# Optimization experiments

Measured on AMD Instinct MI355X. Metric: run time of the kernel, lower is better.

## Reference

```python
import jax, jax.numpy as jnp
import numpy as np


def _lstm_layer(x, Wih, Whh, bih, bhh):
    # x: (B, S, I); Wih: (4H, I); Whh: (4H, H)
    B, S, _ = x.shape
    H = Whh.shape[1]
    # Big batched GEMM for all input projections at once.
    xproj = jnp.einsum('bsi,gi->bsg', x, Wih) + bih + bhh  # (B, S, 4H)
    xproj_t = jnp.transpose(xproj, (1, 0, 2))              # (S, B, 4H)

    def step(carry, xp):
        h, c = carry
        gates = xp + h @ Whh.T                             # (B, 4H)
        i, f, g, o = jnp.split(gates, 4, axis=-1)          # torch gate order i,f,g,o
        i = jax.nn.sigmoid(i)
        f = jax.nn.sigmoid(f)
        g = jnp.tanh(g)
        o = jax.nn.sigmoid(o)
        c = f * c + i * g
        h = o * jnp.tanh(c)
        return (h, c), h

    h0 = jnp.zeros((B, H), dtype=x.dtype)
    c0 = jnp.zeros((B, H), dtype=x.dtype)
    (_, _), hs = jax.lax.scan(step, (h0, c0), xproj_t)     # hs: (S, B, H)
    return jnp.transpose(hs, (1, 0, 2))                    # (B, S, H)


def setup_inputs() -> dict:
    key = jax.random.key(0)
    ks = jax.random.split(key, 12)
    B, S, I, H, O = 64, 512, 512, 1024, 64
    s_in = 1.0 / np.sqrt(H)
    inp = {
        'x': jax.random.normal(ks[0], (B, S, I), dtype=jnp.float32),
        'Wih0': jax.random.uniform(ks[1], (4 * H, I), minval=-s_in, maxval=s_in),
        'Whh0': jax.random.uniform(ks[2], (4 * H, H), minval=-s_in, maxval=s_in),
        'bih0': jax.random.uniform(ks[3], (4 * H,), minval=-s_in, maxval=s_in),
        'bhh0': jax.random.uniform(ks[4], (4 * H,), minval=-s_in, maxval=s_in),
        'Wih1': jax.random.uniform(ks[5], (4 * H, H), minval=-s_in, maxval=s_in),
        'Whh1': jax.random.uniform(ks[6], (4 * H, H), minval=-s_in, maxval=s_in),
        'bih1': jax.random.uniform(ks[7], (4 * H,), minval=-s_in, maxval=s_in),
        'bhh1': jax.random.uniform(ks[8], (4 * H,), minval=-s_in, maxval=s_in),
        'Wfc': jax.random.uniform(ks[9], (O, H), minval=-s_in, maxval=s_in),
        'bfc': jax.random.uniform(ks[10], (O,), minval=-s_in, maxval=s_in),
    }
    return inp


def reference(x, Wih0, Whh0, bih0, bhh0, Wih1, Whh1, bih1, bhh1, Wfc, bfc):
    h = _lstm_layer(x, Wih0, Whh0, bih0, bhh0)   # (B, S, H)
    h = _lstm_layer(h, Wih1, Whh1, bih1, bhh1)   # (B, S, H)
    # dropout = 0.0 (eval mode) -> identity
    logits = jnp.einsum('bsh,oh->bso', h, Wfc) + bfc  # (B, S, O)
    return logits
```

## Files before the change

### kernel.cpp

```cpp
#include <hip/hip_runtime.h>
#include <stdint.h>

typedef _Float16 f16;
typedef _Float16 f16x8 __attribute__((ext_vector_type(8)));
typedef float f32x4 __attribute__((ext_vector_type(4)));

#define MFMA16(a, b, c) __builtin_amdgcn_mfma_f32_16x16x32_f16((a), (b), (c), 0, 0, 0)



__global__ void k_conv_x(const float* __restrict__ x, f16* __restrict__ x16) {
  int i = blockIdx.x * 256 + threadIdx.x;
  int o = i * 8;
  int s = o >> 15, b = (o >> 9) & 63, c = o & 511;
  const float* src = x + (size_t)b * 262144 + (size_t)s * 512 + c;
  float4 v0 = *(const float4*)(src);
  float4 v1 = *(const float4*)(src + 4);
  union { f16 h[8]; f16x8 v; } t;
  t.h[0] = (f16)v0.x; t.h[1] = (f16)v0.y; t.h[2] = (f16)v0.z; t.h[3] = (f16)v0.w;
  t.h[4] = (f16)v1.x; t.h[5] = (f16)v1.y; t.h[6] = (f16)v1.z; t.h[7] = (f16)v1.w;
  *(f16x8*)(x16 + o) = t.v;
}

__global__ void k_conv_wfrag(const float* __restrict__ Wih, const float* __restrict__ Whh,
                             f16* __restrict__ Wf, int KI, int KK, int kPer) {
  int fid = blockIdx.x;
  int lane = threadIdx.x;
  int cf = fid & 1; int rest = fid >> 1;
  int kk = rest % KK; rest /= KK; int w = rest & 7; int jb = rest >> 3;
  int c = cf * 16 + (lane & 15);
  int g = (c >> 3) * 1024 + jb * 8 + (c & 7);
  int k = w * kPer + kk * 32 + ((lane >> 4) << 3);
  const float* src = (k < KI) ? (Wih + (size_t)g * KI + k)
                              : (Whh + (size_t)g * 1024 + (k - KI));
  union { f16 h[8]; f16x8 v; } t;
#pragma unroll
  for (int i = 0; i < 8; ++i) t.h[i] = (f16)src[i];
  *(f16x8*)(Wf + ((size_t)fid * 64 + lane) * 8) = t.v;
}

__global__ void k_conv_bias(const float* __restrict__ bih, const float* __restrict__ bhh,
                            float* __restrict__ br) {
  int d = blockIdx.x * 64 + threadIdx.x;
  int jb = d >> 5, r = d & 31;
  int g = (r >> 3) * 1024 + jb * 8 + (r & 7);
  br[d] = bih[g] + bhh[g];
}

__global__ void k_conv_wfc(const float* __restrict__ Wfc, f16* __restrict__ Wfc16) {
  int i = blockIdx.x * 256 + threadIdx.x;
  Wfc16[i] = (f16)Wfc[i];
}

__global__ __launch_bounds__(512, 2)
void k_persist(const f16* __restrict__ x16,
               const f16* __restrict__ W0f, const float* __restrict__ b0r,
               const f16* __restrict__ W1f, const float* __restrict__ b1r,
               f16* __restrict__ h0buf, f16* __restrict__ h1buf,
               f16* __restrict__ h1all, int* flags, int* gflags) {
  const int layer = blockIdx.x >> 7;
  const int jb = blockIdx.x & 127;

  __shared__ float cred[8][64][36];

  int* flag0 = flags;
  int* flag1 = flags + 4096;
  int* myflag = (layer ? flag1 : flag0) + jb * 32;

  const int tid = threadIdx.x;
  const int w = tid >> 6, lane = tid & 63;
  const int l15 = lane & 15, q8 = (lane >> 4) << 3;
  const int m = tid >> 3, jl = tid & 7, jg = jb * 8 + jl;

  const float* bias = (layer ? b1r : b0r) + jb * 32;
  const float bI = bias[jl], bF = bias[8 + jl], bG = bias[16 + jl], bO = bias[24 + jl];
  float creg = 0.f;

  const int* gp = gflags + l15;
  const bool isg1 = l15 >= 8;
  const int* aggp = (layer ? flag1 : flag0) + (jb * 16 + l15) * 32;
  int* myg = gflags + (layer ? 8 : 0) + jb;

#define POLLG(n0v, n1v)                                                                  \
  {                                                                                      \
    int need_ = isg1 ? (n1v) : (n0v);                                                    \
    if (w == 0) {                                                                        \
      for (;;) {                                                                         \
        int v_ = __hip_atomic_load(gp, __ATOMIC_RELAXED, __HIP_MEMORY_SCOPE_AGENT);      \
        if (__all(v_ >= need_)) break;                                                   \
        __builtin_amdgcn_s_sleep(2);                                                     \
      }                                                                                  \
    }                                                                                    \
    __syncthreads();                                                                     \
  }

#define CRED_AND_POINTWISE(HOUT, HALL)                                                   \
  {                                                                                      \
    _Pragma("unroll") for (int rf = 0; rf < 4; ++rf)                                     \
      _Pragma("unroll") for (int cf = 0; cf < 2; ++cf)                                   \
        _Pragma("unroll") for (int r = 0; r < 4; ++r)                                    \
          cred[w][rf * 16 + (lane >> 4) * 4 + r][cf * 16 + l15] = acc[rf][cf][r];        \
    __syncthreads();                                                                     \
    float ip = bI, fp = bF, gp2 = bG, op = bO;                                           \
    _Pragma("unroll") for (int ww = 0; ww < 8; ++ww) {                                   \
      ip += cred[ww][m][jl];                                                             \
      fp += cred[ww][m][8 + jl];                                                         \
      gp2 += cred[ww][m][16 + jl];                                                       \
      op += cred[ww][m][24 + jl];                                                        \
    }                                                                                    \
    float ig = 1.f / (1.f + __expf(-ip));                                                \
    float fg = 1.f / (1.f + __expf(-fp));                                                \
    float ea = __expf(-2.f * fabsf(gp2));                                                \
    float gg = copysignf((1.f - ea) / (1.f + ea), gp2);                                  \
    float og = 1.f / (1.f + __expf(-op));                                                \
    creg = fg * creg + ig * gg;                                                          \
    float eb = __expf(-2.f * fabsf(creg));                                               \
    float hval = og * copysignf((1.f - eb) / (1.f + eb), creg);                          \
    size_t idx = (size_t)m * 1024 + jg;                                                  \
    union { f16 h; unsigned short s; } cv; cv.h = (f16)hval;                             \
    __hip_atomic_store((unsigned short*)((HOUT) + idx), cv.s,                            \
                       __ATOMIC_RELAXED, __HIP_MEMORY_SCOPE_AGENT);                      \
    if (HALL) ((f16*)(HALL))[idx] = cv.h;                                                \
    __syncthreads();                         \
    if (tid == 0)                                                                        \
      __hip_atomic_store(myflag, t + 1, __ATOMIC_RELAXED, __HIP_MEMORY_SCOPE_AGENT);     \
    if (jb < 8 && w == 0) {                                                              \
      for (;;) {                                                                         \
        int v_ = __hip_atomic_load(aggp, __ATOMIC_RELAXED, __HIP_MEMORY_SCOPE_AGENT);    \
        if (__all(v_ >= t + 1)) break;                                                   \
        __builtin_amdgcn_s_sleep(1);                                                     \
      }                                                                                  \
      if (lane == 0)                                                                     \
        __hip_atomic_store(myg, t + 1, __ATOMIC_RELAXED, __HIP_MEMORY_SCOPE_AGENT);      \
    }                                                                                    \
  }

#define GLD_X(dst, addr)                                                                 \
  asm volatile("global_load_dwordx4 %0, %1, off sc0 sc1" : "=&v"(dst) : "v"(addr) : "memory")
#define GLD_C(dst, addr)                                                                 \
  asm volatile("global_load_dwordx4 %0, %1, off" : "=&v"(dst) : "v"(addr) : "memory")
#define WAITV(n)                                                                         \
  { asm volatile("s_waitcnt vmcnt(" #n ")" ::: "memory"); __builtin_amdgcn_sched_barrier(0); }

  if (layer == 0) {
    const int KK = 6;
    f16x8 wreg[6][2];
#pragma unroll
    for (int kk = 0; kk < KK; ++kk)
#pragma unroll
      for (int cf = 0; cf < 2; ++cf)
        wreg[kk][cf] = *(const f16x8*)(W0f + ((size_t)((jb * 8 + w) * KK + kk) * 2 + cf) * 512 + lane * 8);
#pragma unroll
    for (int kk = 0; kk < KK; ++kk)
      asm volatile("" : "+v"(wreg[kk][0]), "+v"(wreg[kk][1]));

    const int kbeg = w * 192;
    for (int t = 0; t < 512; ++t) {
      const f16* A0 = x16 + (size_t)t * 32768;
      const f16* A1 = h0buf + (size_t)((t + 3) & 3) * 65536;
      f16* hout = h0buf + (size_t)(t & 3) * 65536;

      POLLG(t, t - 3);

      f16x8 af[4][4];
#define ISSUE0(kk)                                                                       \
      {                                                                                  \
        int k_ = kbeg + (kk) * 32 + q8;                                                  \
        if (k_ < 512) {                                                                  \
          const f16* ap_ = A0 + k_;                                                      \
          _Pragma("unroll") for (int rf = 0; rf < 4; ++rf)                               \
            GLD_C(af[(kk) & 3][rf], ap_ + (size_t)(rf * 16 + l15) * 512);                \
        } else {                                                                         \
          const f16* ap_ = A1 + (k_ - 512);                                              \
          _Pragma("unroll") for (int rf = 0; rf < 4; ++rf)                               \
            GLD_X(af[(kk) & 3][rf], ap_ + (size_t)(rf * 16 + l15) * 1024);               \
        }                                                                                \
      }
#define MF0(kk)                                                                          \
      { _Pragma("unroll") for (int rf = 0; rf < 4; ++rf) {                               \
          acc[rf][0] = MFMA16(af[(kk) & 3][rf], wreg[kk][0], acc[rf][0]);                \
          acc[rf][1] = MFMA16(af[(kk) & 3][rf], wreg[kk][1], acc[rf][1]); } }

      f32x4 acc[4][2];
#pragma unroll
      for (int i = 0; i < 4; ++i) {
        acc[i][0] = f32x4{0.f, 0.f, 0.f, 0.f};
        acc[i][1] = f32x4{0.f, 0.f, 0.f, 0.f};
      }

      ISSUE0(0) ISSUE0(1) ISSUE0(2) ISSUE0(3)
      WAITV(12) MF0(0) ISSUE0(4)
      WAITV(12) MF0(1) ISSUE0(5)
      WAITV(12) MF0(2)
      WAITV(8)  MF0(3)
      WAITV(4)  MF0(4)
      WAITV(0)  MF0(5)
#undef ISSUE0
#undef MF0

      CRED_AND_POINTWISE(hout, (f16*)nullptr);
    }
  } else {
    const int KK = 8;
    f16x8 wreg[8][2];
#pragma unroll
    for (int kk = 0; kk < KK; ++kk)
#pragma unroll
      for (int cf = 0; cf < 2; ++cf)
        wreg[kk][cf] = *(const f16x8*)(W1f + ((size_t)((jb * 8 + w) * KK + kk) * 2 + cf) * 512 + lane * 8);
#pragma unroll
    for (int kk = 0; kk < KK; ++kk)
      asm volatile("" : "+v"(wreg[kk][0]), "+v"(wreg[kk][1]));

    const int kbeg = w * 256;
    for (int t = 0; t < 512; ++t) {
      const f16* A0 = h0buf + (size_t)(t & 3) * 65536;
      const f16* A1 = h1buf + (size_t)((t + 3) & 3) * 65536;
      f16* hout = h1buf + (size_t)(t & 3) * 65536;
      f16* hall = h1all + (size_t)t * 65536;

      POLLG(t + 1, t);

      f16x8 af[4][4];
#define ISSUE1(kk)                                                                       \
      {                                                                                  \
        int k_ = kbeg + (kk) * 32 + q8;                                                  \
        const f16* ap_ = (k_ < 1024) ? (A0 + k_) : (A1 + (k_ - 1024));                   \
        _Pragma("unroll") for (int rf = 0; rf < 4; ++rf)                                 \
          GLD_X(af[(kk) & 3][rf], ap_ + (size_t)(rf * 16 + l15) * 1024);                 \
      }
#define MF1(kk)                                                                          \
      { _Pragma("unroll") for (int rf = 0; rf < 4; ++rf) {                               \
          acc[rf][0] = MFMA16(af[(kk) & 3][rf], wreg[kk][0], acc[rf][0]);                \
          acc[rf][1] = MFMA16(af[(kk) & 3][rf], wreg[kk][1], acc[rf][1]); } }

      f32x4 acc[4][2];
#pragma unroll
      for (int i = 0; i < 4; ++i) {
        acc[i][0] = f32x4{0.f, 0.f, 0.f, 0.f};
        acc[i][1] = f32x4{0.f, 0.f, 0.f, 0.f};
      }

      ISSUE1(0) ISSUE1(1) ISSUE1(2) ISSUE1(3)
      WAITV(12) MF1(0) ISSUE1(4)
      WAITV(12) MF1(1) ISSUE1(5)
      WAITV(12) MF1(2) ISSUE1(6)
      WAITV(12) MF1(3) ISSUE1(7)
      WAITV(12) MF1(4)
      WAITV(8)  MF1(5)
      WAITV(4)  MF1(6)
      WAITV(0)  MF1(7)
#undef ISSUE1
#undef MF1

      CRED_AND_POINTWISE(hout, hall);
    }
  }
#undef POLLG
#undef CRED_AND_POINTWISE
#undef GLD_X
#undef GLD_C
#undef WAITV
}

__global__ __launch_bounds__(512, 1)
void k_fc(const f16* __restrict__ h1all, const f16* __restrict__ Wfc16,
          const float* __restrict__ bfc, float* __restrict__ out) {
  const int s = blockIdx.x;
  const f16* A = h1all + (size_t)s * 65536;
  __shared__ float credf[8][64][68];

  const int w = threadIdx.x >> 6;
  const int lane = threadIdx.x & 63;
  const int l15 = lane & 15;
  const int ksub = (lane >> 4) << 3;

  f32x4 acc[4][4];
#pragma unroll
  for (int i = 0; i < 4; ++i)
#pragma unroll
    for (int j = 0; j < 4; ++j) acc[i][j] = f32x4{0.f, 0.f, 0.f, 0.f};

  const int kbeg = w * 128, kend = kbeg + 128;
  f16x8 af0[4], bf0[4], af1[4], bf1[4];

  auto LOADK = [&](int kc, f16x8(&a)[4], f16x8(&b)[4]) {
    const f16* ap = A + kc + ksub;
#pragma unroll
    for (int rf = 0; rf < 4; ++rf)
      a[rf] = *(const f16x8*)(ap + (size_t)(rf * 16 + l15) * 1024);
    const f16* bp = Wfc16 + kc + ksub;
#pragma unroll
    for (int cf = 0; cf < 4; ++cf)
      b[cf] = *(const f16x8*)(bp + (size_t)(cf * 16 + l15) * 1024);
  };

  LOADK(kbeg, af0, bf0);
  for (int kc = kbeg; kc < kend; kc += 64) {
    LOADK(kc + 32, af1, bf1);
#pragma unroll
    for (int rf = 0; rf < 4; ++rf)
#pragma unroll
      for (int cf = 0; cf < 4; ++cf) acc[rf][cf] = MFMA16(af0[rf], bf0[cf], acc[rf][cf]);
    if (kc + 64 < kend) LOADK(kc + 64, af0, bf0);
#pragma unroll
    for (int rf = 0; rf < 4; ++rf)
#pragma unroll
      for (int cf = 0; cf < 4; ++cf) acc[rf][cf] = MFMA16(af1[rf], bf1[cf], acc[rf][cf]);
  }

#pragma unroll
  for (int rf = 0; rf < 4; ++rf)
#pragma unroll
    for (int cf = 0; cf < 4; ++cf)
#pragma unroll
      for (int r = 0; r < 4; ++r)
        credf[w][rf * 16 + (lane >> 4) * 4 + r][cf * 16 + l15] = acc[rf][cf][r];

  __syncthreads();

  int m = threadIdx.x >> 3;
  int cbase = (threadIdx.x & 7) * 8;
#pragma unroll
  for (int u = 0; u < 8; ++u) {
    int col = cbase + u;
    float v = bfc[col];
#pragma unroll
    for (int ww = 0; ww < 8; ++ww) v += credf[ww][m][col];
    out[((size_t)m * 512 + s) * 64 + col] = v;
  }
}

extern "C" void kernel_launch(void* const* d_in, const int* in_sizes, int n_in,
                              void* d_out, int out_size, void* d_ws, size_t ws_size,
                              hipStream_t stream) {
  const float* x    = (const float*)d_in[0];
  const float* Wih0 = (const float*)d_in[1];
  const float* Whh0 = (const float*)d_in[2];
  const float* bih0 = (const float*)d_in[3];
  const float* bhh0 = (const float*)d_in[4];
  const float* Wih1 = (const float*)d_in[5];
  const float* Whh1 = (const float*)d_in[6];
  const float* bih1 = (const float*)d_in[7];
  const float* bhh1 = (const float*)d_in[8];
  const float* Wfc  = (const float*)d_in[9];
  const float* bfc  = (const float*)d_in[10];
  float* out = (float*)d_out;

  char* ws = (char*)d_ws;
  f16*   W0f   = (f16*)(ws + 0);
  f16*   W1f   = (f16*)(ws + 12582912);
  f16*   Wfc16 = (f16*)(ws + 29360128);
  float* b0r   = (float*)(ws + 29491200);
  float* b1r   = (float*)(ws + 29507584);
  f16*   x16   = (f16*)(ws + 29523968);
  f16*   h1all = (f16*)(ws + 63078400);
  f16*   h0buf = (f16*)(ws + 130187264);
  f16*   h1buf = (f16*)(ws + 130711552);
  int*   flags = (int*)(ws + 131235840);
  int*   gfl   = (int*)(ws + 131268608);

  k_conv_x<<<8192, 256, 0, stream>>>(x, x16);
  k_conv_wfrag<<<12288, 64, 0, stream>>>(Wih0, Whh0, W0f, 512, 6, 192);
  k_conv_wfrag<<<16384, 64, 0, stream>>>(Wih1, Whh1, W1f, 1024, 8, 256);
  k_conv_bias<<<64, 64, 0, stream>>>(bih0, bhh0, b0r);
  k_conv_bias<<<64, 64, 0, stream>>>(bih1, bhh1, b1r);
  k_conv_wfc<<<256, 256, 0, stream>>>(Wfc, Wfc16);
  hipMemsetAsync(ws + 130187264, 0, 524288 * 2 + 32768 + 64, stream);

  {
    const f16* x16c = x16; const f16* W0fc = W0f; const float* b0rc = b0r;
    const f16* W1fc = W1f; const float* b1rc = b1r;
    f16 *p0 = h0buf, *p1 = h1buf, *ph = h1all;
    int* fl = flags; int* gf = gfl;
    void* kargs[] = { &x16c, &W0fc, &b0rc, &W1fc, &b1rc, &p0, &p1, &ph, &fl, &gf };
    hipLaunchCooperativeKernel((void*)k_persist, dim3(256), dim3(512), kargs, 0, stream);
  }

  k_fc<<<512, 512, 0, stream>>>(h1all, Wfc16, bfc, out);
}
```

Baseline: 5.467 ms.

## Replace two-level flag aggregation with direct polling of packed per-block flags

Removes the hierarchical gflag aggregation, in which 8 blocks per layer waited on 16 others and republished. Per-block flags are now packed contiguously (256 ints), and each poller wave reads all 256 flags with four coalesced loads per iteration. Layer-0 waves 0-2 also issue their x-projection loads before polling, since those loads do not depend on h, so they overlap with the wait. This cuts one hop of synchronisation latency per timestep, at the cost of every block polling 256 flags, which adds L2 traffic.

```diff
diff --git a/kernel.cpp b/kernel.cpp
--- a/kernel.cpp
+++ b/kernel.cpp
@@ -57,15 +57,13 @@
                const f16* __restrict__ W0f, const float* __restrict__ b0r,
                const f16* __restrict__ W1f, const float* __restrict__ b1r,
                f16* __restrict__ h0buf, f16* __restrict__ h1buf,
-               f16* __restrict__ h1all, int* flags, int* gflags) {
+               f16* __restrict__ h1all, int* flags) {
   const int layer = blockIdx.x >> 7;
   const int jb = blockIdx.x & 127;
 
   __shared__ float cred[8][64][36];
 
-  int* flag0 = flags;
-  int* flag1 = flags + 4096;
-  int* myflag = (layer ? flag1 : flag0) + jb * 32;
+  int* myflag = flags + layer * 128 + jb;
 
   const int tid = threadIdx.x;
   const int w = tid >> 6, lane = tid & 63;
@@ -76,19 +74,28 @@
   const float bI = bias[jl], bF = bias[8 + jl], bG = bias[16 + jl], bO = bias[24 + jl];
   float creg = 0.f;
 
-  const int* gp = gflags + l15;
-  const bool isg1 = l15 >= 8;
-  const int* aggp = (layer ? flag1 : flag0) + (jb * 16 + l15) * 32;
-  int* myg = gflags + (layer ? 8 : 0) + jb;
+  const int* pf0a = flags + lane;
+  const int* pf0b = flags + 64 + lane;
+  const int* pf1a = flags + 128 + lane;
+  const int* pf1b = flags + 192 + lane;
 
 #define POLLG(n0v, n1v)                                                                  \
   {                                                                                      \
-    int need_ = isg1 ? (n1v) : (n0v);                                                    \
     if (w == 0) {                                                                        \
+      int n0 = (n0v), n1 = (n1v);                                                        \
       for (;;) {                                                                         \
-        int v_ = __hip_atomic_load(gp, __ATOMIC_RELAXED, __HIP_MEMORY_SCOPE_AGENT);      \
-        if (__all(v_ >= need_)) break;                                                   \
-        __builtin_amdgcn_s_sleep(2);                                                     \
+        int a_, b_, c_, d_;                                                              \
+        asm volatile(                                                                    \
+            "global_load_dword %0, %4, off sc0 sc1\n\t"                                  \
+            "global_load_dword %1, %5, off sc0 sc1\n\t"                                  \
+            "global_load_dword %2, %6, off sc0 sc1\n\t"                                  \
+            "global_load_dword %3, %7, off sc0 sc1\n\t"                                  \
+            "s_waitcnt vmcnt(0)"                                                         \
+            : "=&v"(a_), "=&v"(b_), "=&v"(c_), "=&v"(d_)                                 \
+            : "v"(pf0a), "v"(pf0b), "v"(pf1a), "v"(pf1b)                                 \
+            : "memory");                                                                 \
+        if (__all((a_ >= n0) && (b_ >= n0) && (c_ >= n1) && (d_ >= n1))) break;          \
+        __builtin_amdgcn_s_sleep(1);                                                     \
       }                                                                                  \
     }                                                                                    \
     __syncthreads();                                                                     \
@@ -124,15 +131,6 @@
     __syncthreads();                         \
     if (tid == 0)                                                                        \
       __hip_atomic_store(myflag, t + 1, __ATOMIC_RELAXED, __HIP_MEMORY_SCOPE_AGENT);     \
-    if (jb < 8 && w == 0) {                                                              \
-      for (;;) {                                                                         \
-        int v_ = __hip_atomic_load(aggp, __ATOMIC_RELAXED, __HIP_MEMORY_SCOPE_AGENT);    \
-        if (__all(v_ >= t + 1)) break;                                                   \
-        __builtin_amdgcn_s_sleep(1);                                                     \
-      }                                                                                  \
-      if (lane == 0)                                                                     \
-        __hip_atomic_store(myg, t + 1, __ATOMIC_RELAXED, __HIP_MEMORY_SCOPE_AGENT);      \
-    }                                                                                    \
   }
 
 #define GLD_X(dst, addr)                                                                 \
@@ -159,8 +157,6 @@
       const f16* A0 = x16 + (size_t)t * 32768;
       const f16* A1 = h0buf + (size_t)((t + 3) & 3) * 65536;
       f16* hout = h0buf + (size_t)(t & 3) * 65536;
-
-      POLLG(t, t - 3);
 
       f16x8 af[4][4];
 #define ISSUE0(kk)                                                                       \
@@ -188,7 +184,9 @@
         acc[i][1] = f32x4{0.f, 0.f, 0.f, 0.f};
       }
 
-      ISSUE0(0) ISSUE0(1) ISSUE0(2) ISSUE0(3)
+      if (w <= 2) { ISSUE0(0) ISSUE0(1) ISSUE0(2) ISSUE0(3) }
+      POLLG(t, t - 3);
+      if (w > 2) { ISSUE0(0) ISSUE0(1) ISSUE0(2) ISSUE0(3) }
       WAITV(12) MF0(0) ISSUE0(4)
       WAITV(12) MF0(1) ISSUE0(5)
       WAITV(12) MF0(2)
@@ -358,7 +356,6 @@
   f16*   h0buf = (f16*)(ws + 130187264);
   f16*   h1buf = (f16*)(ws + 130711552);
   int*   flags = (int*)(ws + 131235840);
-  int*   gfl   = (int*)(ws + 131268608);
 
   k_conv_x<<<8192, 256, 0, stream>>>(x, x16);
   k_conv_wfrag<<<12288, 64, 0, stream>>>(Wih0, Whh0, W0f, 512, 6, 192);
@@ -366,14 +363,14 @@
   k_conv_bias<<<64, 64, 0, stream>>>(bih0, bhh0, b0r);
   k_conv_bias<<<64, 64, 0, stream>>>(bih1, bhh1, b1r);
   k_conv_wfc<<<256, 256, 0, stream>>>(Wfc, Wfc16);
-  hipMemsetAsync(ws + 130187264, 0, 524288 * 2 + 32768 + 64, stream);
+  hipMemsetAsync(ws + 130187264, 0, 524288 * 2 + 1024, stream);
 
   {
     const f16* x16c = x16; const f16* W0fc = W0f; const float* b0rc = b0r;
     const f16* W1fc = W1f; const float* b1rc = b1r;
     f16 *p0 = h0buf, *p1 = h1buf, *ph = h1all;
-    int* fl = flags; int* gf = gfl;
-    void* kargs[] = { &x16c, &W0fc, &b0rc, &W1fc, &b1rc, &p0, &p1, &ph, &fl, &gf };
+    int* fl = flags;
+    void* kargs[] = { &x16c, &W0fc, &b0rc, &W1fc, &b1rc, &p0, &p1, &ph, &fl };
     hipLaunchCooperativeKernel((void*)k_persist, dim3(256), dim3(512), kargs, 0, stream);
   }
 
```

After: 6.211 ms. +13.6%, slower.

## Store hidden states in full-sequence rings to allow cached loads and drop extra writes

Applied to the files above, without the earlier changes.

Replaces the 4-slot rotating hidden-state buffers with append-only rings indexed by timestep. Layer 1 writes each h directly into its full-history ring, so the separate h1all copy store goes away and the FC kernel reads from the ring. Because a slot is never overwritten, reads of completed hidden states can use the cached load path instead of the cache-bypassing one. When the workspace is large enough, layer 0 also gets a full ring and no longer waits on a lag condition from layer 1. The poll sleep interval is also shortened. This uses more workspace and relies on cached loads seeing the writes made by other blocks.

```diff
diff --git a/kernel.cpp b/kernel.cpp
--- a/kernel.cpp
+++ b/kernel.cpp
@@ -52,12 +52,13 @@
   Wfc16[i] = (f16)Wfc[i];
 }
 
+template <int H0C>
 __global__ __launch_bounds__(512, 2)
 void k_persist(const f16* __restrict__ x16,
                const f16* __restrict__ W0f, const float* __restrict__ b0r,
                const f16* __restrict__ W1f, const float* __restrict__ b1r,
-               f16* __restrict__ h0buf, f16* __restrict__ h1buf,
-               f16* __restrict__ h1all, int* flags, int* gflags) {
+               f16* __restrict__ h0ring, f16* __restrict__ h1ring,
+               int* flags, int* gflags) {
   const int layer = blockIdx.x >> 7;
   const int jb = blockIdx.x & 127;
 
@@ -88,13 +89,13 @@
       for (;;) {                                                                         \
         int v_ = __hip_atomic_load(gp, __ATOMIC_RELAXED, __HIP_MEMORY_SCOPE_AGENT);      \
         if (__all(v_ >= need_)) break;                                                   \
-        __builtin_amdgcn_s_sleep(2);                                                     \
+        __builtin_amdgcn_s_sleep(1);                                                     \
       }                                                                                  \
     }                                                                                    \
     __syncthreads();                                                                     \
   }
 
-#define CRED_AND_POINTWISE(HOUT, HALL)                                                   \
+#define CRED_AND_POINTWISE(HOUT)                                                         \
   {                                                                                      \
     _Pragma("unroll") for (int rf = 0; rf < 4; ++rf)                                     \
       _Pragma("unroll") for (int cf = 0; cf < 2; ++cf)                                   \
@@ -120,8 +121,7 @@
     union { f16 h; unsigned short s; } cv; cv.h = (f16)hval;                             \
     __hip_atomic_store((unsigned short*)((HOUT) + idx), cv.s,                            \
                        __ATOMIC_RELAXED, __HIP_MEMORY_SCOPE_AGENT);                      \
-    if (HALL) ((f16*)(HALL))[idx] = cv.h;                                                \
-    __syncthreads();                         \
+    __syncthreads();                          \
     if (tid == 0)                                                                        \
       __hip_atomic_store(myflag, t + 1, __ATOMIC_RELAXED, __HIP_MEMORY_SCOPE_AGENT);     \
     if (jb < 8 && w == 0) {                                                              \
@@ -156,24 +156,28 @@
 
     const int kbeg = w * 192;
     for (int t = 0; t < 512; ++t) {
-      const f16* A0 = x16 + (size_t)t * 32768;
-      const f16* A1 = h0buf + (size_t)((t + 3) & 3) * 65536;
-      f16* hout = h0buf + (size_t)(t & 3) * 65536;
-
-      POLLG(t, t - 3);
+      const f16* A0x = x16 + (size_t)t * 32768;
+      const f16* A1h = H0C ? (h0ring + (size_t)t * 65536)
+                           : (h0ring + (size_t)((t + 3) & 3) * 65536);
+      f16* hout = H0C ? (h0ring + (size_t)(t + 1) * 65536)
+                      : (h0ring + (size_t)(t & 3) * 65536);
+
+      POLLG(t, H0C ? 0 : (t - 3));
 
       f16x8 af[4][4];
 #define ISSUE0(kk)                                                                       \
       {                                                                                  \
         int k_ = kbeg + (kk) * 32 + q8;                                                  \
         if (k_ < 512) {                                                                  \
-          const f16* ap_ = A0 + k_;                                                      \
+          const f16* ap_ = A0x + k_;                                                     \
           _Pragma("unroll") for (int rf = 0; rf < 4; ++rf)                               \
             GLD_C(af[(kk) & 3][rf], ap_ + (size_t)(rf * 16 + l15) * 512);                \
         } else {                                                                         \
-          const f16* ap_ = A1 + (k_ - 512);                                              \
-          _Pragma("unroll") for (int rf = 0; rf < 4; ++rf)                               \
-            GLD_X(af[(kk) & 3][rf], ap_ + (size_t)(rf * 16 + l15) * 1024);               \
+          const f16* ap_ = A1h + (k_ - 512);                                             \
+          _Pragma("unroll") for (int rf = 0; rf < 4; ++rf) {                             \
+            if (H0C) { GLD_C(af[(kk) & 3][rf], ap_ + (size_t)(rf * 16 + l15) * 1024); }  \
+            else     { GLD_X(af[(kk) & 3][rf], ap_ + (size_t)(rf * 16 + l15) * 1024); }  \
+          }                                                                              \
         }                                                                                \
       }
 #define MF0(kk)                                                                          \
@@ -198,7 +202,7 @@
 #undef ISSUE0
 #undef MF0
 
-      CRED_AND_POINTWISE(hout, (f16*)nullptr);
+      CRED_AND_POINTWISE(hout);
     }
   } else {
     const int KK = 8;
@@ -214,10 +218,10 @@
 
     const int kbeg = w * 256;
     for (int t = 0; t < 512; ++t) {
-      const f16* A0 = h0buf + (size_t)(t & 3) * 65536;
-      const f16* A1 = h1buf + (size_t)((t + 3) & 3) * 65536;
-      f16* hout = h1buf + (size_t)(t & 3) * 65536;
-      f16* hall = h1all + (size_t)t * 65536;
+      const f16* A0 = H0C ? (h0ring + (size_t)(t + 1) * 65536)
+                          : (h0ring + (size_t)(t & 3) * 65536);
+      const f16* A1 = h1ring + (size_t)t * 65536;
+      f16* hout = h1ring + (size_t)(t + 1) * 65536;
 
       POLLG(t + 1, t);
 
@@ -225,9 +229,17 @@
 #define ISSUE1(kk)                                                                       \
       {                                                                                  \
         int k_ = kbeg + (kk) * 32 + q8;                                                  \
-        const f16* ap_ = (k_ < 1024) ? (A0 + k_) : (A1 + (k_ - 1024));                   \
-        _Pragma("unroll") for (int rf = 0; rf < 4; ++rf)                                 \
-          GLD_X(af[(kk) & 3][rf], ap_ + (size_t)(rf * 16 + l15) * 1024);                 \
+        if (k_ < 1024) {                                                                 \
+          const f16* ap_ = A0 + k_;                                                      \
+          _Pragma("unroll") for (int rf = 0; rf < 4; ++rf) {                             \
+            if (H0C) { GLD_C(af[(kk) & 3][rf], ap_ + (size_t)(rf * 16 + l15) * 1024); }  \
+            else     { GLD_X(af[(kk) & 3][rf], ap_ + (size_t)(rf * 16 + l15) * 1024); }  \
+          }                                                                              \
+        } else {                                                                         \
+          const f16* ap_ = A1 + (k_ - 1024);                                             \
+          _Pragma("unroll") for (int rf = 0; rf < 4; ++rf)                               \
+            GLD_C(af[(kk) & 3][rf], ap_ + (size_t)(rf * 16 + l15) * 1024);               \
+        }                                                                                \
       }
 #define MF1(kk)                                                                          \
       { _Pragma("unroll") for (int rf = 0; rf < 4; ++rf) {                               \
@@ -253,7 +265,7 @@
 #undef ISSUE1
 #undef MF1
 
-      CRED_AND_POINTWISE(hout, hall);
+      CRED_AND_POINTWISE(hout);
     }
   }
 #undef POLLG
@@ -354,11 +366,26 @@
   float* b0r   = (float*)(ws + 29491200);
   float* b1r   = (float*)(ws + 29507584);
   f16*   x16   = (f16*)(ws + 29523968);
-  f16*   h1all = (f16*)(ws + 63078400);
-  f16*   h0buf = (f16*)(ws + 130187264);
-  f16*   h1buf = (f16*)(ws + 130711552);
-  int*   flags = (int*)(ws + 131235840);
-  int*   gfl   = (int*)(ws + 131268608);
+
+  const size_t H0OFF = 63078400;
+  const size_t SLOT = 131072;
+  const bool big = ws_size >= (size_t)197591104;
+
+  f16 *h0ring, *h1ring;
+  size_t h1off, floff;
+  if (big) {
+    h0ring = (f16*)(ws + H0OFF);
+    h1off = H0OFF + 513 * SLOT;
+    h1ring = (f16*)(ws + h1off);
+    floff = h1off + 513 * SLOT;
+  } else {
+    h0ring = (f16*)(ws + H0OFF);
+    h1off = H0OFF + 4 * SLOT;
+    h1ring = (f16*)(ws + h1off);
+    floff = h1off + 513 * SLOT;
+  }
+  int* flags = (int*)(ws + floff);
+  int* gfl   = (int*)(ws + floff + 32768);
 
   k_conv_x<<<8192, 256, 0, stream>>>(x, x16);
   k_conv_wfrag<<<12288, 64, 0, stream>>>(Wih0, Whh0, W0f, 512, 6, 192);
@@ -366,16 +393,25 @@
   k_conv_bias<<<64, 64, 0, stream>>>(bih0, bhh0, b0r);
   k_conv_bias<<<64, 64, 0, stream>>>(bih1, bhh1, b1r);
   k_conv_wfc<<<256, 256, 0, stream>>>(Wfc, Wfc16);
-  hipMemsetAsync(ws + 130187264, 0, 524288 * 2 + 32768 + 64, stream);
+  if (big) {
+    hipMemsetAsync(ws + H0OFF, 0, SLOT, stream);
+  } else {
+    hipMemsetAsync(ws + H0OFF, 0, 4 * SLOT, stream);
+  }
+  hipMemsetAsync(ws + h1off, 0, SLOT, stream);
+  hipMemsetAsync(ws + floff, 0, 32768 + 64, stream);
 
   {
     const f16* x16c = x16; const f16* W0fc = W0f; const float* b0rc = b0r;
     const f16* W1fc = W1f; const float* b1rc = b1r;
-    f16 *p0 = h0buf, *p1 = h1buf, *ph = h1all;
+    f16 *p0 = h0ring, *p1 = h1ring;
     int* fl = flags; int* gf = gfl;
-    void* kargs[] = { &x16c, &W0fc, &b0rc, &W1fc, &b1rc, &p0, &p1, &ph, &fl, &gf };
-    hipLaunchCooperativeKernel((void*)k_persist, dim3(256), dim3(512), kargs, 0, stream);
-  }
-
-  k_fc<<<512, 512, 0, stream>>>(h1all, Wfc16, bfc, out);
-}
+    void* kargs[] = { &x16c, &W0fc, &b0rc, &W1fc, &b1rc, &p0, &p1, &fl, &gf };
+    if (big)
+      hipLaunchCooperativeKernel((void*)(&k_persist<1>), dim3(256), dim3(512), kargs, 0, stream);
+    else
+      hipLaunchCooperativeKernel((void*)(&k_persist<0>), dim3(256), dim3(512), kargs, 0, stream);
+  }
+
+  k_fc<<<512, 512, 0, stream>>>(h1ring + 65536, Wfc16, bfc, out);
+}
```

After: 5.754 ms. 5.2% more time.
